# Performance work log

Hardware: AMD Instinct MI355X
Metric: run time of the kernel (lower is better)

Reference implementation:

```python
import jax, jax.numpy as jnp
import numpy as np

N_NODES = 50000
E_RAW = 1600000
EMB_DIM = 32
HID = 128
OUT = 128


def setup_inputs() -> dict:
    key = jax.random.key(0)
    k1, k2, k3, k4, k5, k6 = jax.random.split(key, 6)
    x = jnp.arange(N_NODES, dtype=jnp.int64)
    edge_index = jax.random.randint(k1, (2, E_RAW), 0, N_NODES, dtype=jnp.int64)
    emb = jax.random.normal(k2, (N_NODES, EMB_DIM), dtype=jnp.float32)
    W1 = jax.random.normal(k3, (EMB_DIM, HID), dtype=jnp.float32) / np.sqrt(EMB_DIM)
    b1 = jnp.zeros((HID,), dtype=jnp.float32)
    W2 = jax.random.normal(k4, (HID, OUT), dtype=jnp.float32) / np.sqrt(HID)
    b2 = jnp.zeros((OUT,), dtype=jnp.float32)
    return {"x": x, "edge_index": edge_index, "emb": emb,
            "W1": W1, "b1": b1, "W2": W2, "b2": b2}


def _gcn_norm(edge_index, num_nodes):
    # add self-loops, then symmetric normalization deg^-1/2 A_hat deg^-1/2
    loop = jnp.arange(num_nodes, dtype=edge_index.dtype)
    src = jnp.concatenate([edge_index[0], loop])
    dst = jnp.concatenate([edge_index[1], loop])
    ones = jnp.ones(src.shape[0], dtype=jnp.float32)
    deg = jax.ops.segment_sum(ones, dst, num_segments=num_nodes)
    dinv = jax.lax.rsqrt(deg)  # deg >= 1 due to self-loops
    norm = dinv[src] * dinv[dst]  # [E+N]
    return src, dst, norm


def _gcn_conv(h, src, dst, norm, W, b, num_nodes):
    h = h @ W                                  # [N, d_out] dense GEMM
    msg = h[src] * norm[:, None]               # gather + edge scale
    agg = jax.ops.segment_sum(msg, dst, num_segments=num_nodes)  # scatter-add
    return agg + b


def reference(x, edge_index, emb, W1, b1, W2, b2):
    num_nodes = emb.shape[0]
    h = emb[x]                                 # embedding lookup
    src, dst, norm = _gcn_norm(edge_index, num_nodes)
    h = _gcn_conv(h, src, dst, norm, W1, b1, num_nodes)
    h = jax.nn.relu(h)
    out = _gcn_conv(h, src, dst, norm, W2, b2, num_nodes)
    return out
```

## Files before the change

kernel.cpp:

```cpp
#include <hip/hip_runtime.h>


#define NPP   6250
#define NC    32

typedef unsigned short vushort4 __attribute__((ext_vector_type(4)));

static inline int cdiv(int a, int b){ return (a + b - 1) / b; }

__device__ __forceinline__ unsigned short f2bf(float f){
    unsigned int u = __float_as_uint(f);
    u += 0x7fffu + ((u >> 16) & 1u);
    return (unsigned short)(u >> 16);
}
__device__ __forceinline__ float bf2f(unsigned short b){
    return __uint_as_float(((unsigned int)b) << 16);
}
__device__ __forceinline__ void nt_store_u4(unsigned short* p, const ushort4& v){
    vushort4 t = {v.x, v.y, v.z, v.w};
    __builtin_nontemporal_store(t, (vushort4*)p);
}

__global__ __launch_bounds__(256) void k_bucket(const int* __restrict__ src,
        const int* __restrict__ dst, int E, int* __restrict__ staged,
        int* __restrict__ gcur, int npp, int C){
    __shared__ int qcnt[8];
    __shared__ int qbase[8];
    __shared__ int qbuf[8 * 256];
    int tid = threadIdx.x;
    if (tid < 8) qcnt[tid] = 0;
    __syncthreads();
    int e0 = blockIdx.x * 1024 + tid * 4;
    if (e0 + 3 < E){
        int4 d4 = *(const int4*)(dst + e0);
        int4 s4 = *(const int4*)(src + e0);
        int dd[4] = {d4.x, d4.y, d4.z, d4.w};
        int ss[4] = {s4.x, s4.y, s4.z, s4.w};
        #pragma unroll
        for (int i = 0; i < 4; i++){
            int p = dd[i] / npp;
            int pk = ((dd[i] - p * npp) << 17) | ss[i];
            int pos = atomicAdd(&qcnt[p], 1);
            if (pos < 256) qbuf[p * 256 + pos] = pk;
            else {
                int gp = atomicAdd(&gcur[p], 1);
                staged[(size_t)p * C + gp] = pk;
            }
        }
    } else {
        for (int e = e0; e < E && e < e0 + 4; e++){
            int d = dst[e], s = src[e];
            int p = d / npp;
            int pk = ((d - p * npp) << 17) | s;
            int pos = atomicAdd(&qcnt[p], 1);
            if (pos < 256) qbuf[p * 256 + pos] = pk;
            else {
                int gp = atomicAdd(&gcur[p], 1);
                staged[(size_t)p * C + gp] = pk;
            }
        }
    }
    __syncthreads();
    if (tid < 8){
        int nq = min(qcnt[tid], 256);
        qbase[tid] = (nq > 0) ? atomicAdd(&gcur[tid], nq) : 0;
    }
    __syncthreads();
    for (int b = 0; b < 8; b++){
        int nq = min(qcnt[b], 256);
        int gb = qbase[b];
        for (int i = tid; i < nq; i += 256)
            staged[(size_t)b * C + gb + i] = qbuf[b * 256 + i];
    }
}

__global__ __launch_bounds__(256) void k_hist(const int* __restrict__ staged,
        const int* __restrict__ gcur, int C, int CH, int npp,
        unsigned short* __restrict__ H){
    __shared__ int hist[NPP];
    int part  = blockIdx.x & 7;
    int chunk = blockIdx.x >> 3;
    int tid = threadIdx.x;
    for (int i = tid; i < npp; i += 256) hist[i] = 0;
    __syncthreads();
    int pc = gcur[part];
    int e0 = chunk * CH, e1 = min(e0 + CH, pc);
    const int* sd = staged + (size_t)part * C;
    for (int e = e0 + tid; e < e1; e += 256)
        atomicAdd(&hist[(unsigned)sd[e] >> 17], 1);
    __syncthreads();
    unsigned short* Hrow = H + (size_t)(part * NC + chunk) * npp;
    for (int i = tid; i < npp; i += 256) Hrow[i] = (unsigned short)hist[i];
}

__global__ __launch_bounds__(256) void k_nodescan(unsigned short* __restrict__ H,
        int npp, int n, int* __restrict__ ecount, float* __restrict__ dinv,
        int* __restrict__ bsum, const float* __restrict__ emb,
        const int* __restrict__ x, unsigned short* __restrict__ es){
    __shared__ int s[256];
    int t = blockIdx.x * 256 + threadIdx.x;
    int run = 0;
    if (t < 8 * npp && t < n){
        int p  = t / npp;
        int dl = t - p * npp;
        #pragma unroll
        for (int c = 0; c < NC; c++){
            size_t idx = (size_t)(p * NC + c) * npp + dl;
            int v = H[idx];
            H[idx] = (unsigned short)run;
            run += v;
        }
        ecount[t] = run;
        float dv = rsqrtf((float)run + 1.0f);
        dinv[t] = dv;
        const float* er = emb + (size_t)x[t] * 32;
        #pragma unroll
        for (int c4 = 0; c4 < 32; c4 += 4){
            float4 v = *(const float4*)(er + c4);
            ushort4 o;
            o.x = f2bf(v.x * dv); o.y = f2bf(v.y * dv);
            o.z = f2bf(v.z * dv); o.w = f2bf(v.w * dv);
            *(ushort4*)(es + (size_t)t * 32 + c4) = o;
        }
    }
    s[threadIdx.x] = run;
    __syncthreads();
    for (int d = 128; d > 0; d >>= 1){
        if (threadIdx.x < d) s[threadIdx.x] += s[threadIdx.x + d];
        __syncthreads();
    }
    if (threadIdx.x == 0) bsum[blockIdx.x] = s[0];
}

__global__ __launch_bounds__(256) void k_scanBC(const int* __restrict__ ecount, int n,
        const int* __restrict__ bsum, int nb, int* __restrict__ offsets){
    __shared__ int bs[256];
    __shared__ int s[256];
    int t = threadIdx.x;
    bs[t] = (t < nb) ? bsum[t] : 0;
    __syncthreads();
    if (t == 0){
        int run = 0;
        for (int b = 0; b < nb; b++){ int v = bs[b]; bs[b] = run; run += v; }
    }
    __syncthreads();
    int i = blockIdx.x * 256 + t;
    int v = (i < n) ? ecount[i] : 0;
    s[t] = v;
    __syncthreads();
    for (int d = 1; d < 256; d <<= 1){
        int x2 = (t >= d) ? s[t - d] : 0;
        __syncthreads();
        s[t] += x2;
        __syncthreads();
    }
    if (i < n) offsets[i] = bs[blockIdx.x] + s[t] - v;
}

__global__ __launch_bounds__(256) void k_fill3(const int* __restrict__ staged,
        const int* __restrict__ gcur, int C, int CH, int npp,
        const unsigned short* __restrict__ H, const int* __restrict__ offsets,
        int* __restrict__ csr_src){
    __shared__ int cur[NPP];
    int part  = blockIdx.x & 7;
    int chunk = blockIdx.x >> 3;
    int tid = threadIdx.x;
    const unsigned short* Hrow = H + (size_t)(part * NC + chunk) * npp;
    for (int i = tid; i < npp; i += 256) cur[i] = Hrow[i];
    __syncthreads();
    int pc = gcur[part];
    int lo = part * npp;
    int e0 = chunk * CH, e1 = min(e0 + CH, pc);
    const int* sd = staged + (size_t)part * C;
    for (int e = e0 + tid; e < e1; e += 256){
        int pk = sd[e];
        int dl = (unsigned)pk >> 17;
        int r = atomicAdd(&cur[dl], 1);
        csr_src[offsets[lo + dl] + r] = pk & 0x1FFFF;
    }
}

__global__ __launch_bounds__(256) void k_l1(const unsigned short* __restrict__ es,
        const int* __restrict__ offsets, const int* __restrict__ ecount,
        const int* __restrict__ csr, const float* __restrict__ dinv,
        const float* __restrict__ W1, const float* __restrict__ b1,
        unsigned short* __restrict__ hs, int n){
    __shared__ float w[32 * 128];
    __shared__ float a1t[8][32];
    for (int i = threadIdx.x; i < 32 * 128; i += 256) w[i] = W1[i];
    int g    = threadIdx.x >> 5;
    int lane = threadIdx.x & 31;
    int node = blockIdx.x * 8 + g;
    if (node < n){
        int off = offsets[node], cnt = ecount[node];
        float s0 = bf2f(es[(size_t)node * 32 + lane]);
        float s1 = 0.f;
        int e = 0;
        for (; e + 16 <= cnt; e += 16){
            int idx[16];
            #pragma unroll
            for (int i = 0; i < 16; i++) idx[i] = __builtin_nontemporal_load(csr + off + e + i);
            unsigned short v[16];
            #pragma unroll
            for (int i = 0; i < 16; i++) v[i] = es[(size_t)idx[i] * 32 + lane];
            #pragma unroll
            for (int i = 0; i < 16; i += 2){
                s0 += bf2f(v[i]);
                s1 += bf2f(v[i + 1]);
            }
        }
        for (; e + 8 <= cnt; e += 8){
            int idx[8];
            #pragma unroll
            for (int i = 0; i < 8; i++) idx[i] = __builtin_nontemporal_load(csr + off + e + i);
            unsigned short v[8];
            #pragma unroll
            for (int i = 0; i < 8; i++) v[i] = es[(size_t)idx[i] * 32 + lane];
            #pragma unroll
            for (int i = 0; i < 8; i += 2){
                s0 += bf2f(v[i]);
                s1 += bf2f(v[i + 1]);
            }
        }
        for (; e < cnt; e++)
            s0 += bf2f(es[(size_t)__builtin_nontemporal_load(csr + off + e) * 32 + lane]);
        a1t[g][lane] = dinv[node] * (s0 + s1);
    }
    __syncthreads();
    if (node >= n) return;
    int c4 = lane * 4;
    float4 acc = *(const float4*)(b1 + c4);
    #pragma unroll
    for (int k4 = 0; k4 < 8; k4++){
        float4 av = *(const float4*)&a1t[g][k4 * 4];
        float4 w0 = *(const float4*)&w[(k4 * 4 + 0) * 128 + c4];
        float4 w1 = *(const float4*)&w[(k4 * 4 + 1) * 128 + c4];
        float4 w2 = *(const float4*)&w[(k4 * 4 + 2) * 128 + c4];
        float4 w3 = *(const float4*)&w[(k4 * 4 + 3) * 128 + c4];
        acc.x += av.x * w0.x + av.y * w1.x + av.z * w2.x + av.w * w3.x;
        acc.y += av.x * w0.y + av.y * w1.y + av.z * w2.y + av.w * w3.y;
        acc.z += av.x * w0.z + av.y * w1.z + av.z * w2.z + av.w * w3.z;
        acc.w += av.x * w0.w + av.y * w1.w + av.z * w2.w + av.w * w3.w;
    }
    float dv = dinv[node];
    ushort4 o;
    o.x = f2bf(dv * fmaxf(acc.x, 0.f));
    o.y = f2bf(dv * fmaxf(acc.y, 0.f));
    o.z = f2bf(dv * fmaxf(acc.z, 0.f));
    o.w = f2bf(dv * fmaxf(acc.w, 0.f));
    nt_store_u4(hs + (size_t)node * 128 + c4, o);
}

__global__ __launch_bounds__(256) void k_l2(const unsigned short* __restrict__ hs,
        const int* __restrict__ offsets, const int* __restrict__ ecount,
        const int* __restrict__ csr, const float* __restrict__ dinv,
        const float* __restrict__ W2, const float* __restrict__ b2,
        float* __restrict__ out, int n){
    __shared__ float a2t[32 * 128];
    int g    = threadIdx.x >> 5;
    int lane = threadIdx.x & 31;
    int c4g  = lane * 4;
    #pragma unroll
    for (int j = 0; j < 4; j++){
        int nl = g + 8 * j;
        int node = blockIdx.x * 32 + nl;
        if (node < n){
            int off = offsets[node], cnt = ecount[node];
            ushort4 sv = *(const ushort4*)(hs + (size_t)node * 128 + c4g);
            float ax0 = bf2f(sv.x), ax1 = 0.f;
            float ay0 = bf2f(sv.y), ay1 = 0.f;
            float az0 = bf2f(sv.z), az1 = 0.f;
            float aw0 = bf2f(sv.w), aw1 = 0.f;
            int e = 0;
            for (; e + 8 <= cnt; e += 8){
                int i0 = csr[off + e + 0], i1 = csr[off + e + 1];
                int i2 = csr[off + e + 2], i3 = csr[off + e + 3];
                int i4 = csr[off + e + 4], i5 = csr[off + e + 5];
                int i6 = csr[off + e + 6], i7 = csr[off + e + 7];
                ushort4 v0 = *(const ushort4*)(hs + (size_t)i0 * 128 + c4g);
                ushort4 v1 = *(const ushort4*)(hs + (size_t)i1 * 128 + c4g);
                ushort4 v2 = *(const ushort4*)(hs + (size_t)i2 * 128 + c4g);
                ushort4 v3 = *(const ushort4*)(hs + (size_t)i3 * 128 + c4g);
                ushort4 v4 = *(const ushort4*)(hs + (size_t)i4 * 128 + c4g);
                ushort4 v5 = *(const ushort4*)(hs + (size_t)i5 * 128 + c4g);
                ushort4 v6 = *(const ushort4*)(hs + (size_t)i6 * 128 + c4g);
                ushort4 v7 = *(const ushort4*)(hs + (size_t)i7 * 128 + c4g);
                ax0 += bf2f(v0.x) + bf2f(v2.x) + bf2f(v4.x) + bf2f(v6.x);
                ax1 += bf2f(v1.x) + bf2f(v3.x) + bf2f(v5.x) + bf2f(v7.x);
                ay0 += bf2f(v0.y) + bf2f(v2.y) + bf2f(v4.y) + bf2f(v6.y);
                ay1 += bf2f(v1.y) + bf2f(v3.y) + bf2f(v5.y) + bf2f(v7.y);
                az0 += bf2f(v0.z) + bf2f(v2.z) + bf2f(v4.z) + bf2f(v6.z);
                az1 += bf2f(v1.z) + bf2f(v3.z) + bf2f(v5.z) + bf2f(v7.z);
                aw0 += bf2f(v0.w) + bf2f(v2.w) + bf2f(v4.w) + bf2f(v6.w);
                aw1 += bf2f(v1.w) + bf2f(v3.w) + bf2f(v5.w) + bf2f(v7.w);
            }
            for (; e < cnt; e++){
                ushort4 v = *(const ushort4*)(hs + (size_t)csr[off + e] * 128 + c4g);
                ax0 += bf2f(v.x); ay0 += bf2f(v.y); az0 += bf2f(v.z); aw0 += bf2f(v.w);
            }
            float dv = dinv[node];
            float4 r;
            r.x = dv * (ax0 + ax1); r.y = dv * (ay0 + ay1);
            r.z = dv * (az0 + az1); r.w = dv * (aw0 + aw1);
            *(float4*)&a2t[nl * 128 + c4g] = r;
        }
    }
    __syncthreads();
    int c4 = lane * 4;
    int r0 = (threadIdx.x >> 5) * 4;
    float4 bias = *(const float4*)(b2 + c4);
    float4 acc0 = bias, acc1 = bias, acc2 = bias, acc3 = bias;
    for (int k = 0; k < 128; k += 4){
        float4 a0  = *(const float4*)&a2t[(r0 + 0) * 128 + k];
        float4 a1v = *(const float4*)&a2t[(r0 + 1) * 128 + k];
        float4 a2v = *(const float4*)&a2t[(r0 + 2) * 128 + k];
        float4 a3v = *(const float4*)&a2t[(r0 + 3) * 128 + k];
        #pragma unroll
        for (int kk = 0; kk < 4; kk++){
            float4 wv = *(const float4*)(W2 + (size_t)(k + kk) * 128 + c4);
            float b0 = (kk == 0) ? a0.x  : (kk == 1) ? a0.y  : (kk == 2) ? a0.z  : a0.w;
            float b1v= (kk == 0) ? a1v.x : (kk == 1) ? a1v.y : (kk == 2) ? a1v.z : a1v.w;
            float b2v= (kk == 0) ? a2v.x : (kk == 1) ? a2v.y : (kk == 2) ? a2v.z : a2v.w;
            float b3 = (kk == 0) ? a3v.x : (kk == 1) ? a3v.y : (kk == 2) ? a3v.z : a3v.w;
            acc0.x += b0 * wv.x; acc0.y += b0 * wv.y; acc0.z += b0 * wv.z; acc0.w += b0 * wv.w;
            acc1.x += b1v * wv.x; acc1.y += b1v * wv.y; acc1.z += b1v * wv.z; acc1.w += b1v * wv.w;
            acc2.x += b2v * wv.x; acc2.y += b2v * wv.y; acc2.z += b2v * wv.z; acc2.w += b2v * wv.w;
            acc3.x += b3 * wv.x; acc3.y += b3 * wv.y; acc3.z += b3 * wv.z; acc3.w += b3 * wv.w;
        }
    }
    int rb = blockIdx.x * 32 + r0;
    if (rb + 0 < n) *(float4*)(out + (size_t)(rb + 0) * 128 + c4) = acc0;
    if (rb + 1 < n) *(float4*)(out + (size_t)(rb + 1) * 128 + c4) = acc1;
    if (rb + 2 < n) *(float4*)(out + (size_t)(rb + 2) * 128 + c4) = acc2;
    if (rb + 3 < n) *(float4*)(out + (size_t)(rb + 3) * 128 + c4) = acc3;
}

extern "C" void kernel_launch(void* const* d_in, const int* in_sizes, int n_in,
                              void* d_out, int out_size, void* d_ws, size_t ws_size,
                              hipStream_t stream){
    const int*   x    = (const int*)d_in[0];
    const int*   ei   = (const int*)d_in[1];
    const float* emb  = (const float*)d_in[2];
    const float* W1   = (const float*)d_in[3];
    const float* b1   = (const float*)d_in[4];
    const float* W2   = (const float*)d_in[5];
    const float* b2   = (const float*)d_in[6];
    const int N = in_sizes[0];
    const int E = in_sizes[1] / 2;
    const int* srcv = ei;
    const int* dstv = ei + E;
    float* out = (float*)d_out;

    char* p = (char*)d_ws;
    auto alloc = [&](size_t bytes) -> char* {
        char* r = p; p += (bytes + 255) & ~(size_t)255; return r;
    };
    int nb = cdiv(N, 256);
    int*            ecount  = (int*)           alloc((size_t)(N + 8) * 4);
    int*            gcur    = ecount + N;
    int*            offsets = (int*)           alloc((size_t)N * 4);
    int*            bsum    = (int*)           alloc((size_t)nb * 4);
    float*          dinv    = (float*)         alloc((size_t)N * 4);
    int*            csr     = (int*)           alloc((size_t)E * 4);
    unsigned short* es      = (unsigned short*)alloc((size_t)N * 32 * 2);
    unsigned short* H       = (unsigned short*)alloc((size_t)8 * NC * NPP * 2);
    unsigned short* hs      = (unsigned short*)alloc((size_t)N * 128 * 2);
    int*            staged  = (int*)           alloc((size_t)(E + 8 * 65536) * 4);
    (void)ws_size; (void)n_in; (void)out_size;

    const int npp = cdiv(N, 8);
    const int C   = E / 8 + 65536;
    const int CH  = cdiv(C, NC);

    hipMemsetAsync(gcur, 0, 8 * sizeof(int), stream);
    k_bucket  <<<cdiv(E, 1024), 256, 0, stream>>>(srcv, dstv, E, staged, gcur, npp, C);
    k_hist    <<<8 * NC, 256, 0, stream>>>(staged, gcur, C, CH, npp, H);
    k_nodescan<<<nb, 256, 0, stream>>>(H, npp, N, ecount, dinv, bsum, emb, x, es);
    k_scanBC  <<<nb, 256, 0, stream>>>(ecount, N, bsum, nb, offsets);
    k_fill3   <<<8 * NC, 256, 0, stream>>>(staged, gcur, C, CH, npp, H, offsets, csr);

    k_l1    <<<cdiv(N, 8), 256, 0, stream>>>(es, offsets, ecount, csr, dinv, W1, b1, hs, N);

    k_l2    <<<cdiv(N, 32), 256, 0, stream>>>(hs, offsets, ecount, csr, dinv, W2, b2, out, N);
}
```

Measured before the change: 271.2 us.

## Replace partitioned LDS bucketing CSR build with direct global-atomic degree count and fill

Replaces the partition-bucket, LDS-histogram and chunked fill pipeline with a simpler CSR build. One kernel counts in-degrees with global atomics, a scan produces offsets and a cursor copy, and a fill kernel scatters src ids using global atomics on the cursor. Nontemporal loads and stores in the layer-1 kernel are also reverted to plain accesses. This removes the staging buffer and two passes, but it puts heavy global atomic contention on random destination nodes and produces a nondeterministic neighbour order within each row.

After: 400.7 us. +47.8%, slower.

```diff
diff --git a/kernel.cpp b/kernel.cpp
--- a/kernel.cpp
+++ b/kernel.cpp
@@ -1,10 +1,7 @@
 #include <hip/hip_runtime.h>
 
 
-#define NPP   6250
 #define NC    32
-
-typedef unsigned short vushort4 __attribute__((ext_vector_type(4)));
 
 static inline int cdiv(int a, int b){ return (a + b - 1) / b; }
 
@@ -16,101 +13,31 @@
 __device__ __forceinline__ float bf2f(unsigned short b){
     return __uint_as_float(((unsigned int)b) << 16);
 }
-__device__ __forceinline__ void nt_store_u4(unsigned short* p, const ushort4& v){
-    vushort4 t = {v.x, v.y, v.z, v.w};
-    __builtin_nontemporal_store(t, (vushort4*)p);
-}
-
-__global__ __launch_bounds__(256) void k_bucket(const int* __restrict__ src,
-        const int* __restrict__ dst, int E, int* __restrict__ staged,
-        int* __restrict__ gcur, int npp, int C){
-    __shared__ int qcnt[8];
-    __shared__ int qbase[8];
-    __shared__ int qbuf[8 * 256];
-    int tid = threadIdx.x;
-    if (tid < 8) qcnt[tid] = 0;
-    __syncthreads();
-    int e0 = blockIdx.x * 1024 + tid * 4;
+
+__global__ __launch_bounds__(256) void k_deg(const int* __restrict__ dst, int E,
+        int* __restrict__ ecount){
+    int e0 = blockIdx.x * 1024 + threadIdx.x * 4;
     if (e0 + 3 < E){
         int4 d4 = *(const int4*)(dst + e0);
-        int4 s4 = *(const int4*)(src + e0);
-        int dd[4] = {d4.x, d4.y, d4.z, d4.w};
-        int ss[4] = {s4.x, s4.y, s4.z, s4.w};
-        #pragma unroll
-        for (int i = 0; i < 4; i++){
-            int p = dd[i] / npp;
-            int pk = ((dd[i] - p * npp) << 17) | ss[i];
-            int pos = atomicAdd(&qcnt[p], 1);
-            if (pos < 256) qbuf[p * 256 + pos] = pk;
-            else {
-                int gp = atomicAdd(&gcur[p], 1);
-                staged[(size_t)p * C + gp] = pk;
-            }
-        }
+        atomicAdd(&ecount[d4.x], 1);
+        atomicAdd(&ecount[d4.y], 1);
+        atomicAdd(&ecount[d4.z], 1);
+        atomicAdd(&ecount[d4.w], 1);
     } else {
-        for (int e = e0; e < E && e < e0 + 4; e++){
-            int d = dst[e], s = src[e];
-            int p = d / npp;
-            int pk = ((d - p * npp) << 17) | s;
-            int pos = atomicAdd(&qcnt[p], 1);
-            if (pos < 256) qbuf[p * 256 + pos] = pk;
-            else {
-                int gp = atomicAdd(&gcur[p], 1);
-                staged[(size_t)p * C + gp] = pk;
-            }
-        }
-    }
-    __syncthreads();
-    if (tid < 8){
-        int nq = min(qcnt[tid], 256);
-        qbase[tid] = (nq > 0) ? atomicAdd(&gcur[tid], nq) : 0;
-    }
-    __syncthreads();
-    for (int b = 0; b < 8; b++){
-        int nq = min(qcnt[b], 256);
-        int gb = qbase[b];
-        for (int i = tid; i < nq; i += 256)
-            staged[(size_t)b * C + gb + i] = qbuf[b * 256 + i];
-    }
-}
-
-__global__ __launch_bounds__(256) void k_hist(const int* __restrict__ staged,
-        const int* __restrict__ gcur, int C, int CH, int npp,
-        unsigned short* __restrict__ H){
-    __shared__ int hist[NPP];
-    int part  = blockIdx.x & 7;
-    int chunk = blockIdx.x >> 3;
-    int tid = threadIdx.x;
-    for (int i = tid; i < npp; i += 256) hist[i] = 0;
-    __syncthreads();
-    int pc = gcur[part];
-    int e0 = chunk * CH, e1 = min(e0 + CH, pc);
-    const int* sd = staged + (size_t)part * C;
-    for (int e = e0 + tid; e < e1; e += 256)
-        atomicAdd(&hist[(unsigned)sd[e] >> 17], 1);
-    __syncthreads();
-    unsigned short* Hrow = H + (size_t)(part * NC + chunk) * npp;
-    for (int i = tid; i < npp; i += 256) Hrow[i] = (unsigned short)hist[i];
-}
-
-__global__ __launch_bounds__(256) void k_nodescan(unsigned short* __restrict__ H,
-        int npp, int n, int* __restrict__ ecount, float* __restrict__ dinv,
-        int* __restrict__ bsum, const float* __restrict__ emb,
-        const int* __restrict__ x, unsigned short* __restrict__ es){
+        for (int e = e0; e < E && e < e0 + 4; e++)
+            atomicAdd(&ecount[dst[e]], 1);
+    }
+}
+
+__global__ __launch_bounds__(256) void k_red(const int* __restrict__ ecount, int n,
+        float* __restrict__ dinv, int* __restrict__ bsum,
+        const float* __restrict__ emb, const int* __restrict__ x,
+        unsigned short* __restrict__ es){
     __shared__ int s[256];
     int t = blockIdx.x * 256 + threadIdx.x;
     int run = 0;
-    if (t < 8 * npp && t < n){
-        int p  = t / npp;
-        int dl = t - p * npp;
-        #pragma unroll
-        for (int c = 0; c < NC; c++){
-            size_t idx = (size_t)(p * NC + c) * npp + dl;
-            int v = H[idx];
-            H[idx] = (unsigned short)run;
-            run += v;
-        }
-        ecount[t] = run;
+    if (t < n){
+        run = ecount[t];
         float dv = rsqrtf((float)run + 1.0f);
         dinv[t] = dv;
         const float* er = emb + (size_t)x[t] * 32;
@@ -133,7 +60,8 @@
 }
 
 __global__ __launch_bounds__(256) void k_scanBC(const int* __restrict__ ecount, int n,
-        const int* __restrict__ bsum, int nb, int* __restrict__ offsets){
+        const int* __restrict__ bsum, int nb, int* __restrict__ offsets,
+        int* __restrict__ cursor){
     __shared__ int bs[256];
     __shared__ int s[256];
     int t = threadIdx.x;
@@ -154,29 +82,29 @@
         s[t] += x2;
         __syncthreads();
     }
-    if (i < n) offsets[i] = bs[blockIdx.x] + s[t] - v;
-}
-
-__global__ __launch_bounds__(256) void k_fill3(const int* __restrict__ staged,
-        const int* __restrict__ gcur, int C, int CH, int npp,
-        const unsigned short* __restrict__ H, const int* __restrict__ offsets,
-        int* __restrict__ csr_src){
-    __shared__ int cur[NPP];
-    int part  = blockIdx.x & 7;
-    int chunk = blockIdx.x >> 3;
-    int tid = threadIdx.x;
-    const unsigned short* Hrow = H + (size_t)(part * NC + chunk) * npp;
-    for (int i = tid; i < npp; i += 256) cur[i] = Hrow[i];
-    __syncthreads();
-    int pc = gcur[part];
-    int lo = part * npp;
-    int e0 = chunk * CH, e1 = min(e0 + CH, pc);
-    const int* sd = staged + (size_t)part * C;
-    for (int e = e0 + tid; e < e1; e += 256){
-        int pk = sd[e];
-        int dl = (unsigned)pk >> 17;
-        int r = atomicAdd(&cur[dl], 1);
-        csr_src[offsets[lo + dl] + r] = pk & 0x1FFFF;
+    if (i < n){
+        int o = bs[blockIdx.x] + s[t] - v;
+        offsets[i] = o;
+        cursor[i]  = o;
+    }
+}
+
+__global__ __launch_bounds__(256) void k_fill(const int* __restrict__ src,
+        const int* __restrict__ dst, int E, int* __restrict__ cursor,
+        int* __restrict__ csr){
+    int e0 = blockIdx.x * 1024 + threadIdx.x * 4;
+    if (e0 + 3 < E){
+        int4 d4 = *(const int4*)(dst + e0);
+        int4 s4 = *(const int4*)(src + e0);
+        int r0 = atomicAdd(&cursor[d4.x], 1); csr[r0] = s4.x;
+        int r1 = atomicAdd(&cursor[d4.y], 1); csr[r1] = s4.y;
+        int r2 = atomicAdd(&cursor[d4.z], 1); csr[r2] = s4.z;
+        int r3 = atomicAdd(&cursor[d4.w], 1); csr[r3] = s4.w;
+    } else {
+        for (int e = e0; e < E && e < e0 + 4; e++){
+            int r = atomicAdd(&cursor[dst[e]], 1);
+            csr[r] = src[e];
+        }
     }
 }
 
@@ -199,7 +127,7 @@
         for (; e + 16 <= cnt; e += 16){
             int idx[16];
             #pragma unroll
-            for (int i = 0; i < 16; i++) idx[i] = __builtin_nontemporal_load(csr + off + e + i);
+            for (int i = 0; i < 16; i++) idx[i] = csr[off + e + i];
             unsigned short v[16];
             #pragma unroll
             for (int i = 0; i < 16; i++) v[i] = es[(size_t)idx[i] * 32 + lane];
@@ -212,7 +140,7 @@
         for (; e + 8 <= cnt; e += 8){
             int idx[8];
             #pragma unroll
-            for (int i = 0; i < 8; i++) idx[i] = __builtin_nontemporal_load(csr + off + e + i);
+            for (int i = 0; i < 8; i++) idx[i] = csr[off + e + i];
             unsigned short v[8];
             #pragma unroll
             for (int i = 0; i < 8; i++) v[i] = es[(size_t)idx[i] * 32 + lane];
@@ -222,8 +150,7 @@
                 s1 += bf2f(v[i + 1]);
             }
         }
-        for (; e < cnt; e++)
-            s0 += bf2f(es[(size_t)__builtin_nontemporal_load(csr + off + e) * 32 + lane]);
+        for (; e < cnt; e++) s0 += bf2f(es[(size_t)csr[off + e] * 32 + lane]);
         a1t[g][lane] = dinv[node] * (s0 + s1);
     }
     __syncthreads();
@@ -248,7 +175,7 @@
     o.y = f2bf(dv * fmaxf(acc.y, 0.f));
     o.z = f2bf(dv * fmaxf(acc.z, 0.f));
     o.w = f2bf(dv * fmaxf(acc.w, 0.f));
-    nt_store_u4(hs + (size_t)node * 128 + c4, o);
+    *(ushort4*)(hs + (size_t)node * 128 + c4) = o;
 }
 
 __global__ __launch_bounds__(256) void k_l2(const unsigned short* __restrict__ hs,
@@ -356,28 +283,21 @@
         char* r = p; p += (bytes + 255) & ~(size_t)255; return r;
     };
     int nb = cdiv(N, 256);
-    int*            ecount  = (int*)           alloc((size_t)(N + 8) * 4);
-    int*            gcur    = ecount + N;
+    int*            ecount  = (int*)           alloc((size_t)N * 4);
+    int*            cursor  = (int*)           alloc((size_t)N * 4);
     int*            offsets = (int*)           alloc((size_t)N * 4);
     int*            bsum    = (int*)           alloc((size_t)nb * 4);
     float*          dinv    = (float*)         alloc((size_t)N * 4);
     int*            csr     = (int*)           alloc((size_t)E * 4);
     unsigned short* es      = (unsigned short*)alloc((size_t)N * 32 * 2);
-    unsigned short* H       = (unsigned short*)alloc((size_t)8 * NC * NPP * 2);
     unsigned short* hs      = (unsigned short*)alloc((size_t)N * 128 * 2);
-    int*            staged  = (int*)           alloc((size_t)(E + 8 * 65536) * 4);
     (void)ws_size; (void)n_in; (void)out_size;
 
-    const int npp = cdiv(N, 8);
-    const int C   = E / 8 + 65536;
-    const int CH  = cdiv(C, NC);
-
-    hipMemsetAsync(gcur, 0, 8 * sizeof(int), stream);
-    k_bucket  <<<cdiv(E, 1024), 256, 0, stream>>>(srcv, dstv, E, staged, gcur, npp, C);
-    k_hist    <<<8 * NC, 256, 0, stream>>>(staged, gcur, C, CH, npp, H);
-    k_nodescan<<<nb, 256, 0, stream>>>(H, npp, N, ecount, dinv, bsum, emb, x, es);
-    k_scanBC  <<<nb, 256, 0, stream>>>(ecount, N, bsum, nb, offsets);
-    k_fill3   <<<8 * NC, 256, 0, stream>>>(staged, gcur, C, CH, npp, H, offsets, csr);
+    hipMemsetAsync(ecount, 0, (size_t)N * 4, stream);
+    k_deg   <<<cdiv(E, 1024), 256, 0, stream>>>(dstv, E, ecount);
+    k_red   <<<nb, 256, 0, stream>>>(ecount, N, dinv, bsum, emb, x, es);
+    k_scanBC<<<nb, 256, 0, stream>>>(ecount, N, bsum, nb, offsets, cursor);
+    k_fill  <<<cdiv(E, 1024), 256, 0, stream>>>(srcv, dstv, E, cursor, csr);
 
     k_l1    <<<cdiv(N, 8), 256, 0, stream>>>(es, offsets, ecount, csr, dinv, W1, b1, hs, N);
 
```
